# Kernel optimization log

Measured on AMD Instinct MI355X. Metric: run time of the kernel, lower is better.

## Reference

```python
import jax, jax.numpy as jnp
import numpy as np

B, S = 128, 1024
IN_NUM, IN_STATE = 64, 16
FEAT = 256
HID = 512
NUM_CLS = 32
EMB_WORD, EMB_DIM = 32, 4
LN_EPS = 1e-5


def _layer_norm(x):
    mu = jnp.mean(x, axis=-1, keepdims=True)
    var = jnp.var(x, axis=-1, keepdims=True)
    return (x - mu) * jax.lax.rsqrt(var + LN_EPS)


def setup_inputs() -> dict:
    key = jax.random.key(0)
    ks = jax.random.split(key, 20)
    w = lambda k, shape: jax.random.normal(k, shape, dtype=jnp.float32) * 0.05
    inp = {
        'x_num': jax.random.normal(ks[0], (B, S, IN_NUM), dtype=jnp.float32),
        'x_state': jax.random.randint(ks[1], (B, S, IN_STATE), 0, EMB_WORD),
        # numeric-branch MLP (2 layers)
        'num_w0': w(ks[2], (FEAT, IN_NUM)), 'num_b0': jnp.zeros((FEAT,), jnp.float32),
        'num_w1': w(ks[3], (FEAT, FEAT)),   'num_b1': jnp.zeros((FEAT,), jnp.float32),
        # state-branch embedding + MLP
        'emb': w(ks[4], (EMB_WORD, EMB_DIM)),
        'st_w0': w(ks[5], (FEAT, IN_STATE * EMB_DIM)), 'st_b0': jnp.zeros((FEAT,), jnp.float32),
        'st_w1': w(ks[6], (FEAT, FEAT)),               'st_b1': jnp.zeros((FEAT,), jnp.float32),
        # LSTM gate weights: input dim = 2*FEAT
        'Wii': w(ks[7], (HID, 2 * FEAT)),  'Whi': w(ks[8], (HID, HID)),
        'Wif': w(ks[9], (HID, 2 * FEAT)),  'Whf': w(ks[10], (HID, HID)),
        'Wig': w(ks[11], (HID, 2 * FEAT)), 'Whg': w(ks[12], (HID, HID)),
        'Wio': w(ks[13], (HID, 2 * FEAT)), 'Who': w(ks[14], (HID, HID)),
        'Bii': jnp.zeros((HID,), jnp.float32), 'Bhi': jnp.zeros((HID,), jnp.float32),
        'Bif': jnp.zeros((HID,), jnp.float32), 'Bhf': jnp.zeros((HID,), jnp.float32),
        'Big': jnp.zeros((HID,), jnp.float32), 'Bhg': jnp.zeros((HID,), jnp.float32),
        'Bio': jnp.zeros((HID,), jnp.float32), 'Bho': jnp.zeros((HID,), jnp.float32),
        'out_w': w(ks[15], (NUM_CLS, HID)), 'out_b': jnp.zeros((NUM_CLS,), jnp.float32),
    }
    return inp


def _forward(x_num, x_state, num_w0, num_b0, num_w1, num_b1, emb,
             st_w0, st_b0, st_w1, st_b1,
             Wii, Whi, Wif, Whf, Wig, Whg, Wio, Who,
             Bii, Bhi, Bif, Bhf, Big, Bhg, Bio, Bho,
             out_w, out_b):
    b, s = x_num.shape[0], x_num.shape[1]
    # numeric branch: Linear -> relu -> LayerNorm (dropout is identity in eval)
    h = _layer_norm(jax.nn.relu(x_num @ num_w0.T + num_b0))
    h = _layer_norm(jax.nn.relu(h @ num_w1.T + num_b1))
    # state branch: embedding lookup, flatten per step, then MLP
    e = emb[x_state].reshape(b, s, -1)                      # [B,S,IN_STATE*EMB_DIM]
    g = _layer_norm(jax.nn.relu(e @ st_w0.T + st_b0))
    g = _layer_norm(jax.nn.relu(g @ st_w1.T + st_b1))
    x = jnp.concatenate([h, g], axis=2)                     # [B,S,2*FEAT]

    hid = Whi.shape[0]
    h0 = jnp.zeros((b, hid), x.dtype)
    c0 = jnp.zeros((b, hid), x.dtype)

    def step(carry, x_t):
        h_t, c_t = carry
        i_t = jax.nn.sigmoid(x_t @ Wii.T + h_t @ Whi.T + Bii + Bhi)
        f_t = jax.nn.sigmoid(x_t @ Wif.T + h_t @ Whf.T + Bif + Bhf)
        g_t = jnp.tanh(x_t @ Wig.T + h_t @ Whg.T + Big + Bhg)
        o_t = jax.nn.sigmoid(x_t @ Wio.T + h_t @ Who.T + Bio + Bho)
        c_new = f_t * c_t + i_t * g_t
        h_new = o_t * jnp.tanh(c_new)
        return (h_new, c_new), None

    (h_last, _), _ = jax.lax.scan(step, (h0, c0), jnp.swapaxes(x, 0, 1))
    return h_last @ out_w.T + out_b                          # [B, num_cls]


def reference(x_num, x_state, num_w0, num_b0, num_w1, num_b1, emb,
              st_w0, st_b0, st_w1, st_b1,
              Wii, Whi, Wif, Whf, Wig, Whg, Wio, Who,
              Bii, Bhi, Bif, Bhf, Big, Bhg, Bio, Bho,
              out_w, out_b):
    return _forward(x_num, x_state, num_w0, num_b0, num_w1, num_b1, emb,
                    st_w0, st_b0, st_w1, st_b1,
                    Wii, Whi, Wif, Whf, Wig, Whg, Wio, Who,
                    Bii, Bhi, Bif, Bhf, Big, Bhg, Bio, Bho,
                    out_w, out_b)
```

## Files before the change

kernel.cpp:

```cpp
#include <hip/hip_runtime.h>
#include <hip/hip_bf16.h>

typedef __attribute__((ext_vector_type(4))) float f4;
typedef __attribute__((ext_vector_type(4))) float f32x4;
typedef __attribute__((ext_vector_type(8))) short bf16x8;
typedef unsigned long long ull;

#define OFF_XCAT   0ull
#define OFF_WCAT   134217728ull
#define OFF_BIAS   138412032ull
#define OFF_HBUF   138420224ull
#define OFF_FLAG   138682368ull
#define OFF_CTR    138686464ull
#define WS_NEED    138691584ull

__device__ inline unsigned short f2bf(float x){
  unsigned u = __float_as_uint(x);
  unsigned r = (u + 0x7FFFu + ((u >> 16) & 1u)) >> 16;
  return (unsigned short)r;
}
__device__ inline float bf2f(unsigned short s){ return __uint_as_float(((unsigned)s) << 16); }

__global__ void __launch_bounds__(256) diag_write(float* out, float val){
  out[blockIdx.x * 256 + threadIdx.x] = val;
}

__global__ void __launch_bounds__(256) prep_w(
    const float* Wii, const float* Wif, const float* Wig, const float* Wio,
    const float* Whi, const float* Whf, const float* Whg, const float* Who,
    const float* Bii, const float* Bif, const float* Big, const float* Bio,
    const float* Bhi, const float* Bhf, const float* Bhg, const float* Bho,
    unsigned short* Wcat, float* bias_cat){
  int e = blockIdx.x * 256 + threadIdx.x;
  int col = e >> 10, k = e & 1023;
  int u = col >> 2, g = col & 3;
  float v;
  if (k < 512){
    const float* p = (g==0)?Wii:((g==1)?Wif:((g==2)?Wig:Wio));
    v = p[u*512 + k];
  } else {
    const float* p = (g==0)?Whi:((g==1)?Whf:((g==2)?Whg:Who));
    v = p[u*512 + (k-512)];
  }
  Wcat[e] = f2bf(v);
  if (e < 2048){
    int u2 = e >> 2, g2 = e & 3;
    const float* bx = (g2==0)?Bii:((g2==1)?Bif:((g2==2)?Big:Bio));
    const float* bh = (g2==0)?Bhi:((g2==1)?Bhf:((g2==2)?Bhg:Bho));
    bias_cat[e] = bx[u2] + bh[u2];
  }
}

__global__ void __launch_bounds__(256) stageA_fused(
    const float* __restrict__ xnum, const int* __restrict__ xstate,
    const float* __restrict__ emb,
    const float* __restrict__ num_w0, const float* __restrict__ num_b0,
    const float* __restrict__ num_w1, const float* __restrict__ num_b1,
    const float* __restrict__ st_w0,  const float* __restrict__ st_b0,
    const float* __restrict__ st_w1,  const float* __restrict__ st_b1,
    unsigned short* __restrict__ Xcat){
  __shared__ float Wt[32*256];
  __shared__ float xb[16*68];
  __shared__ float h1[16*260];
  int tid = threadIdx.x;
  long tok0 = (long)blockIdx.x * 16;
  int tg = tid >> 6, c4 = tid & 63;

  #pragma unroll 1
  for (int br = 0; br < 2; ++br){
    const float* W0 = br ? st_w0 : num_w0;
    const float* b0 = br ? st_b0 : num_b0;
    const float* W1 = br ? st_w1 : num_w1;
    const float* b1 = br ? st_b1 : num_b1;

    __syncthreads();
    if (br == 0){
      int tk = tid >> 4, q = tid & 15;
      f4 v = *(const f4*)(xnum + (tok0+tk)*64 + q*4);
      float* d = xb + tk*68 + q*4;
      d[0]=v.x; d[1]=v.y; d[2]=v.z; d[3]=v.w;
    } else {
      int tk = tid >> 4, j = tid & 15;
      int idx = xstate[(tok0+tk)*16 + j];
      f4 v = *(const f4*)(emb + idx*4);
      float* d = xb + tk*68 + j*4;
      d[0]=v.x; d[1]=v.y; d[2]=v.z; d[3]=v.w;
    }

    float acc[4][4];
    { f4 bv = *(const f4*)(b0 + c4*4);
      #pragma unroll
      for (int j=0;j<4;j++){ acc[j][0]=bv.x; acc[j][1]=bv.y; acc[j][2]=bv.z; acc[j][3]=bv.w; } }
    for (int kh=0; kh<2; ++kh){
      __syncthreads();
      { int c = tid;
        const f4* src = (const f4*)(W0 + c*64 + kh*32);
        #pragma unroll
        for (int q=0;q<8;q++){
          f4 v = src[q];
          Wt[(q*4+0)*256 + c] = v.x; Wt[(q*4+1)*256 + c] = v.y;
          Wt[(q*4+2)*256 + c] = v.z; Wt[(q*4+3)*256 + c] = v.w;
        }
      }
      __syncthreads();
      for (int kq=0; kq<8; kq++){
        int k0 = kh*32 + kq*4;
        f4 a0 = *(const f4*)(xb + (tg*4+0)*68 + k0);
        f4 a1 = *(const f4*)(xb + (tg*4+1)*68 + k0);
        f4 a2 = *(const f4*)(xb + (tg*4+2)*68 + k0);
        f4 a3 = *(const f4*)(xb + (tg*4+3)*68 + k0);
        f4 w0 = *(const f4*)(Wt + (kq*4+0)*256 + c4*4);
        f4 w1 = *(const f4*)(Wt + (kq*4+1)*256 + c4*4);
        f4 w2 = *(const f4*)(Wt + (kq*4+2)*256 + c4*4);
        f4 w3 = *(const f4*)(Wt + (kq*4+3)*256 + c4*4);
        #pragma unroll
        for (int j=0;j<4;j++){
          f4 a = (j==0)?a0:((j==1)?a1:((j==2)?a2:a3));
          #pragma unroll
          for (int d=0; d<4; d++)
            acc[j][d] += a.x*w0[d] + a.y*w1[d] + a.z*w2[d] + a.w*w3[d];
        }
      }
    }
    #pragma unroll
    for (int j=0;j<4;j++){
      float v0=fmaxf(acc[j][0],0.f), v1=fmaxf(acc[j][1],0.f);
      float v2=fmaxf(acc[j][2],0.f), v3=fmaxf(acc[j][3],0.f);
      float s1 = v0+v1+v2+v3, s2 = v0*v0+v1*v1+v2*v2+v3*v3;
      for (int off=1; off<64; off<<=1){ s1 += __shfl_xor(s1, off); s2 += __shfl_xor(s2, off); }
      float mu = s1 * (1.f/256.f);
      float rs = rsqrtf(s2*(1.f/256.f) - mu*mu + 1e-5f);
      f4 o; o.x=(v0-mu)*rs; o.y=(v1-mu)*rs; o.z=(v2-mu)*rs; o.w=(v3-mu)*rs;
      *(f4*)(h1 + (tg*4+j)*260 + c4*4) = o;
    }

    float ac2[4][4];
    { f4 bv = *(const f4*)(b1 + c4*4);
      #pragma unroll
      for (int j=0;j<4;j++){ ac2[j][0]=bv.x; ac2[j][1]=bv.y; ac2[j][2]=bv.z; ac2[j][3]=bv.w; } }
    for (int kh=0; kh<8; ++kh){
      __syncthreads();
      { int c = tid;
        const f4* src = (const f4*)(W1 + c*256 + kh*32);
        #pragma unroll
        for (int q=0;q<8;q++){
          f4 v = src[q];
          Wt[(q*4+0)*256 + c] = v.x; Wt[(q*4+1)*256 + c] = v.y;
          Wt[(q*4+2)*256 + c] = v.z; Wt[(q*4+3)*256 + c] = v.w;
        }
      }
      __syncthreads();
      for (int kq=0; kq<8; kq++){
        int k0 = kh*32 + kq*4;
        f4 a0 = *(const f4*)(h1 + (tg*4+0)*260 + k0);
        f4 a1 = *(const f4*)(h1 + (tg*4+1)*260 + k0);
        f4 a2 = *(const f4*)(h1 + (tg*4+2)*260 + k0);
        f4 a3 = *(const f4*)(h1 + (tg*4+3)*260 + k0);
        f4 w0 = *(const f4*)(Wt + (kq*4+0)*256 + c4*4);
        f4 w1 = *(const f4*)(Wt + (kq*4+1)*256 + c4*4);
        f4 w2 = *(const f4*)(Wt + (kq*4+2)*256 + c4*4);
        f4 w3 = *(const f4*)(Wt + (kq*4+3)*256 + c4*4);
        #pragma unroll
        for (int j=0;j<4;j++){
          f4 a = (j==0)?a0:((j==1)?a1:((j==2)?a2:a3));
          #pragma unroll
          for (int d=0; d<4; d++)
            ac2[j][d] += a.x*w0[d] + a.y*w1[d] + a.z*w2[d] + a.w*w3[d];
        }
      }
    }
    #pragma unroll
    for (int j=0;j<4;j++){
      float v0=fmaxf(ac2[j][0],0.f), v1=fmaxf(ac2[j][1],0.f);
      float v2=fmaxf(ac2[j][2],0.f), v3=fmaxf(ac2[j][3],0.f);
      float s1 = v0+v1+v2+v3, s2 = v0*v0+v1*v1+v2*v2+v3*v3;
      for (int off=1; off<64; off<<=1){ s1 += __shfl_xor(s1, off); s2 += __shfl_xor(s2, off); }
      float mu = s1 * (1.f/256.f);
      float rs = rsqrtf(s2*(1.f/256.f) - mu*mu + 1e-5f);
      long tok = tok0 + tg*4 + j;
      long bb = tok >> 10, ss = tok & 1023;
      unsigned short* o = Xcat + (ss*128 + bb)*512 + br*256 + c4*4;
      unsigned lo = (unsigned)f2bf((v0-mu)*rs) | ((unsigned)f2bf((v1-mu)*rs) << 16);
      unsigned hi = (unsigned)f2bf((v2-mu)*rs) | ((unsigned)f2bf((v3-mu)*rs) << 16);
      ((unsigned*)o)[0] = lo; ((unsigned*)o)[1] = hi;
    }
  }
}

__global__ void __launch_bounds__(256, 1) lstm_pk(
    const unsigned short* __restrict__ Xcat,
    const unsigned short* __restrict__ Wcat,
    const float* __restrict__ bias_cat,
    unsigned int* __restrict__ hbuf32,
    unsigned int* __restrict__ flags,
    unsigned int* __restrict__ ctr){
  __shared__ __align__(16) char actb[32768];
  __shared__ int okf, sdead;
  int tid = threadIdx.x;
  int lane = tid & 63, w = tid >> 6;
  int g = blockIdx.x & 7, m = blockIdx.x >> 3;

  int colg = 64*m + 16*w + (lane & 15);
  bf16x8 wf[32];
  {
    const bf16x8* wsrc = (const bf16x8*)(Wcat + colg*1024 + (lane>>4)*8);
    #pragma unroll
    for (int s=0;s<32;s++) wf[s] = wsrc[s*4];
  }
  int cb = 64*m + 16*w + 4*(lane>>4);
  f32x4 bias4;
  bias4.x = bias_cat[cb+0]; bias4.y = bias_cat[cb+1];
  bias4.z = bias_cat[cb+2]; bias4.w = bias_cat[cb+3];

  if (tid == 0){
    __hip_atomic_fetch_add(&ctr[255], 1u, __ATOMIC_RELAXED, __HIP_MEMORY_SCOPE_AGENT);
    unsigned v = 0; int it = 0;
    do {
      v = __hip_atomic_load(&ctr[255], __ATOMIC_RELAXED, __HIP_MEMORY_SCOPE_AGENT);
      if (v >= 256u) break;
      __builtin_amdgcn_s_sleep(8);
    } while (++it < 2000000);
    okf = (v >= 256u) ? 1 : 0;
    sdead = 0;
  }
  __syncthreads();
  if (!okf) return;

  float cst = 0.f;
  int r16 = tid >> 4, q16 = tid & 15;
  const unsigned int* fl = flags + g*32;
  unsigned int* myflag = flags + g*32 + m;

  for (int t=0; t<1024; ++t){
    bf16x8 xf[16];
    {
      const bf16x8* xsrc = (const bf16x8*)(Xcat + ((long)t*128 + g*16 + (lane&15))*512 + (lane>>4)*8);
      #pragma unroll
      for (int s=0;s<16;s++) xf[s] = xsrc[s*4];
    }
    f32x4 acc0 = bias4;
    f32x4 acc1; acc1.x=0.f; acc1.y=0.f; acc1.z=0.f; acc1.w=0.f;
    #pragma unroll
    for (int s=0;s<16;s+=2){
      acc0 = __builtin_amdgcn_mfma_f32_16x16x32_bf16(wf[s],   xf[s],   acc0, 0, 0, 0);
      acc1 = __builtin_amdgcn_mfma_f32_16x16x32_bf16(wf[s+1], xf[s+1], acc1, 0, 0, 0);
    }
    if (t > 0 && w == 0){
      unsigned tt = (unsigned)t; int itc = 0;
      for (;;){
        unsigned a = __hip_atomic_load(&fl[lane & 31], __ATOMIC_RELAXED, __HIP_MEMORY_SCOPE_AGENT);
        if (__all((int)(a >= tt))) break;
        if (++itc > 400000){
          if (lane == 0){
            sdead = 1;
            __hip_atomic_store(&ctr[252], tt, __ATOMIC_RELAXED, __HIP_MEMORY_SCOPE_AGENT);
          }
          break;
        }
      }
      asm volatile("" ::: "memory");
    }
    __syncthreads();
    if (*(volatile int*)&sdead) break;
    {
      const ull* hb = (const ull*)hbuf32 + ((long)(t&1)*8 + g)*(16*128) + r16*128 + q16;
      char* hl = actb + (t&1)*16384;
      ull hv[8];
      #pragma unroll
      for (int i=0;i<8;i++)
        hv[i] = __hip_atomic_load(&hb[i*16], __ATOMIC_RELAXED, __HIP_MEMORY_SCOPE_AGENT);
      #pragma unroll
      for (int i=0;i<8;i++){
        int byt = (r16*1024 + q16*8 + i*128) ^ ((r16 & 7) << 4);
        *(ull*)(hl + byt) = hv[i];
      }
    }
    __syncthreads();
    {
      const char* hl = actb + (t&1)*16384;
      #pragma unroll
      for (int s=0;s<16;s+=2){
        int by0 = ((lane&15)*1024 + s*64     + (lane>>4)*16) ^ (((lane&15)&7) << 4);
        int by1 = ((lane&15)*1024 + (s+1)*64 + (lane>>4)*16) ^ (((lane&15)&7) << 4);
        bf16x8 b0 = *(const bf16x8*)(hl + by0);
        bf16x8 b1 = *(const bf16x8*)(hl + by1);
        acc0 = __builtin_amdgcn_mfma_f32_16x16x32_bf16(wf[16+s], b0, acc0, 0, 0, 0);
        acc1 = __builtin_amdgcn_mfma_f32_16x16x32_bf16(wf[17+s], b1, acc1, 0, 0, 0);
      }
    }
    float gi = acc0.x + acc1.x, gf = acc0.y + acc1.y;
    float gg = acc0.z + acc1.z, go = acc0.w + acc1.w;
    float iv = 1.f / (1.f + __expf(-gi));
    float fv = 1.f / (1.f + __expf(-gf));
    float e2 = __expf(-2.f * gg);
    float gv = (1.f - e2) / (1.f + e2);
    float ov = 1.f / (1.f + __expf(-go));
    cst = fv * cst + iv * gv;
    float e2c = __expf(-2.f * cst);
    float hout = ov * (1.f - e2c) / (1.f + e2c);
    {
      unsigned short hb16 = f2bf(hout);
      int partner = __shfl_xor((int)hb16, 16);
      int hi = lane >> 4;
      if ((hi & 1) == 0){
        int ug = 16*m + 4*w + hi;
        int r = lane & 15;
        unsigned pack = (unsigned)hb16 | (((unsigned)partner & 0xFFFFu) << 16);
        unsigned int* dst = hbuf32 + ((long)((t+1)&1)*8 + g)*(16*256) + r*256 + (ug >> 1);
        __hip_atomic_store(dst, pack, __ATOMIC_RELAXED, __HIP_MEMORY_SCOPE_AGENT);
      }
    }
    asm volatile("s_waitcnt vmcnt(0)" ::: "memory");
    __syncthreads();
    if (tid == 0)
      __hip_atomic_store(myflag, (unsigned)(t+1), __ATOMIC_RELAXED, __HIP_MEMORY_SCOPE_AGENT);
  }

  __syncthreads();
  if (tid == 0 && !sdead)
    __hip_atomic_fetch_add(&ctr[251], 1u, __ATOMIC_RELAXED, __HIP_MEMORY_SCOPE_AGENT);
}

__global__ void __launch_bounds__(256) out_gemm(
    const unsigned short* __restrict__ hbuf, const unsigned int* __restrict__ ctr,
    const float* __restrict__ out_w, const float* __restrict__ out_b,
    float* __restrict__ out){
  unsigned done = ctr[251], arriv = ctr[255], dead = ctr[252];
  if (dead != 0u || done != 256u){
    float v = dead ? (20000.f + (float)dead) : (10000.f + (float)arriv);
    if (threadIdx.x < 32) out[blockIdx.x*32 + threadIdx.x] = v;
    return;
  }
  __shared__ float part[8][32];
  int b = blockIdx.x;
  int g = b >> 4, r = b & 15;
  const unsigned short* hrow = hbuf + ((long)g*16 + r)*512;
  int col = threadIdx.x & 31, p = threadIdx.x >> 5;
  float s = 0.f;
  for (int u = p*64; u < p*64 + 64; ++u)
    s += bf2f(hrow[u]) * out_w[col*512 + u];
  part[p][col] = s;
  __syncthreads();
  if (p == 0){
    float t = out_b[col];
    #pragma unroll
    for (int i=0;i<8;i++) t += part[i][col];
    out[b*32 + col] = t;
  }
}

extern "C" void kernel_launch(void* const* d_in, const int* in_sizes, int n_in,
                              void* d_out, int out_size, void* d_ws, size_t ws_size,
                              hipStream_t stream){
  const float* x_num   = (const float*)d_in[0];
  const int*   x_state = (const int*)d_in[1];
  const float* num_w0  = (const float*)d_in[2];
  const float* num_b0  = (const float*)d_in[3];
  const float* num_w1  = (const float*)d_in[4];
  const float* num_b1  = (const float*)d_in[5];
  const float* emb     = (const float*)d_in[6];
  const float* st_w0   = (const float*)d_in[7];
  const float* st_b0   = (const float*)d_in[8];
  const float* st_w1   = (const float*)d_in[9];
  const float* st_b1   = (const float*)d_in[10];
  const float* Wii = (const float*)d_in[11];
  const float* Whi = (const float*)d_in[12];
  const float* Wif = (const float*)d_in[13];
  const float* Whf = (const float*)d_in[14];
  const float* Wig = (const float*)d_in[15];
  const float* Whg = (const float*)d_in[16];
  const float* Wio = (const float*)d_in[17];
  const float* Who = (const float*)d_in[18];
  const float* Bii = (const float*)d_in[19];
  const float* Bhi = (const float*)d_in[20];
  const float* Bif = (const float*)d_in[21];
  const float* Bhf = (const float*)d_in[22];
  const float* Big = (const float*)d_in[23];
  const float* Bhg = (const float*)d_in[24];
  const float* Bio = (const float*)d_in[25];
  const float* Bho = (const float*)d_in[26];
  const float* out_w = (const float*)d_in[27];
  const float* out_b = (const float*)d_in[28];

  float* out = (float*)d_out;

  diag_write<<<16, 256, 0, stream>>>(out, 50000.f);

  if (ws_size < WS_NEED){
    diag_write<<<16, 256, 0, stream>>>(out, 100000.f + (float)(ws_size >> 20));
    return;
  }

  char* ws = (char*)d_ws;
  unsigned short* Xcat = (unsigned short*)(ws + OFF_XCAT);
  unsigned short* Wcat = (unsigned short*)(ws + OFF_WCAT);
  float* bias_cat      = (float*)(ws + OFF_BIAS);
  unsigned int* hbuf32 = (unsigned int*)(ws + OFF_HBUF);
  unsigned int* flags  = (unsigned int*)(ws + OFF_FLAG);
  unsigned int* ctr    = (unsigned int*)(ws + OFF_CTR);

  hipMemsetAsync(ws + OFF_HBUF, 0, 262144 + 4096 + 1024, stream);

  prep_w<<<8192, 256, 0, stream>>>(Wii, Wif, Wig, Wio, Whi, Whf, Whg, Who,
                                   Bii, Bif, Big, Bio, Bhi, Bhf, Bhg, Bho,
                                   Wcat, bias_cat);

  stageA_fused<<<8192, 256, 0, stream>>>(x_num, x_state, emb,
                                         num_w0, num_b0, num_w1, num_b1,
                                         st_w0, st_b0, st_w1, st_b1, Xcat);

  lstm_pk<<<256, 256, 0, stream>>>(Xcat, Wcat, bias_cat, hbuf32, flags, ctr);

  out_gemm<<<128, 256, 0, stream>>>((const unsigned short*)hbuf32, ctr, out_w, out_b, out);
}
```

Before: 5.789 ms.

## Use per-wave flags and prefetch next step's input GEMM off the critical path

```diff
diff --git a/kernel.cpp b/kernel.cpp
--- a/kernel.cpp
+++ b/kernel.cpp
@@ -11,7 +11,7 @@
 #define OFF_BIAS   138412032ull
 #define OFF_HBUF   138420224ull
 #define OFF_FLAG   138682368ull
-#define OFF_CTR    138686464ull
+#define OFF_CTR    138690560ull
 #define WS_NEED    138691584ull
 
 __device__ inline unsigned short f2bf(float x){
@@ -192,7 +192,7 @@
     const unsigned short* __restrict__ Wcat,
     const float* __restrict__ bias_cat,
     unsigned int* __restrict__ hbuf32,
-    unsigned int* __restrict__ flags,
+    ull* __restrict__ flg,
     unsigned int* __restrict__ ctr){
   __shared__ __align__(16) char actb[32768];
   __shared__ int okf, sdead;
@@ -206,6 +206,8 @@
     const bf16x8* wsrc = (const bf16x8*)(Wcat + colg*1024 + (lane>>4)*8);
     #pragma unroll
     for (int s=0;s<32;s++) wf[s] = wsrc[s*4];
+    #pragma unroll
+    for (int s=0;s<32;s++) asm volatile("" : "+v"(wf[s]));
   }
   int cb = 64*m + 16*w + 4*(lane>>4);
   f32x4 bias4;
@@ -228,47 +230,48 @@
 
   float cst = 0.f;
   int r16 = tid >> 4, q16 = tid & 15;
-  const unsigned int* fl = flags + g*32;
-  unsigned int* myflag = flags + g*32 + m;
-
-  for (int t=0; t<1024; ++t){
+  ull* f8 = flg + g*128;
+  unsigned int* myflag = (unsigned int*)(f8 + (m*4 + w));
+
+  f32x4 acc0, acc1;
+  {
     bf16x8 xf[16];
-    {
-      const bf16x8* xsrc = (const bf16x8*)(Xcat + ((long)t*128 + g*16 + (lane&15))*512 + (lane>>4)*8);
-      #pragma unroll
-      for (int s=0;s<16;s++) xf[s] = xsrc[s*4];
-    }
-    f32x4 acc0 = bias4;
-    f32x4 acc1; acc1.x=0.f; acc1.y=0.f; acc1.z=0.f; acc1.w=0.f;
+    const bf16x8* xsrc = (const bf16x8*)(Xcat + ((long)0*128 + g*16 + (lane&15))*512 + (lane>>4)*8);
+    #pragma unroll
+    for (int s=0;s<16;s++) xf[s] = xsrc[s*4];
+    acc0 = bias4;
+    acc1.x=0.f; acc1.y=0.f; acc1.z=0.f; acc1.w=0.f;
     #pragma unroll
     for (int s=0;s<16;s+=2){
       acc0 = __builtin_amdgcn_mfma_f32_16x16x32_bf16(wf[s],   xf[s],   acc0, 0, 0, 0);
       acc1 = __builtin_amdgcn_mfma_f32_16x16x32_bf16(wf[s+1], xf[s+1], acc1, 0, 0, 0);
     }
-    if (t > 0 && w == 0){
+  }
+
+  #pragma unroll 1
+  for (int t=0; t<1024; ++t){
+    if (t > 0){
       unsigned tt = (unsigned)t; int itc = 0;
       for (;;){
-        unsigned a = __hip_atomic_load(&fl[lane & 31], __ATOMIC_RELAXED, __HIP_MEMORY_SCOPE_AGENT);
-        if (__all((int)(a >= tt))) break;
+        unsigned a = __hip_atomic_load((const unsigned int*)(f8 + lane),      __ATOMIC_RELAXED, __HIP_MEMORY_SCOPE_AGENT);
+        unsigned b = __hip_atomic_load((const unsigned int*)(f8 + 64 + lane), __ATOMIC_RELAXED, __HIP_MEMORY_SCOPE_AGENT);
+        if (__all((int)(a >= tt)) && __all((int)(b >= tt))) break;
+        if ((itc & 127) == 127 && *(volatile int*)&sdead) break;
         if (++itc > 400000){
-          if (lane == 0){
-            sdead = 1;
-            __hip_atomic_store(&ctr[252], tt, __ATOMIC_RELAXED, __HIP_MEMORY_SCOPE_AGENT);
-          }
+          *(volatile int*)&sdead = 1;
+          __hip_atomic_store(&ctr[252], tt, __ATOMIC_RELAXED, __HIP_MEMORY_SCOPE_AGENT);
           break;
         }
       }
       asm volatile("" ::: "memory");
     }
-    __syncthreads();
-    if (*(volatile int*)&sdead) break;
     {
       const ull* hb = (const ull*)hbuf32 + ((long)(t&1)*8 + g)*(16*128) + r16*128 + q16;
-      char* hl = actb + (t&1)*16384;
       ull hv[8];
       #pragma unroll
       for (int i=0;i<8;i++)
         hv[i] = __hip_atomic_load(&hb[i*16], __ATOMIC_RELAXED, __HIP_MEMORY_SCOPE_AGENT);
+      char* hl = actb + (t&1)*16384;
       #pragma unroll
       for (int i=0;i<8;i++){
         int byt = (r16*1024 + q16*8 + i*128) ^ ((r16 & 7) << 4);
@@ -276,6 +279,7 @@
       }
     }
     __syncthreads();
+    if (*(volatile int*)&sdead) break;
     {
       const char* hl = actb + (t&1)*16384;
       #pragma unroll
@@ -311,9 +315,22 @@
       }
     }
     asm volatile("s_waitcnt vmcnt(0)" ::: "memory");
-    __syncthreads();
-    if (tid == 0)
+    if (lane == 0)
       __hip_atomic_store(myflag, (unsigned)(t+1), __ATOMIC_RELAXED, __HIP_MEMORY_SCOPE_AGENT);
+    {
+      int tn = (t < 1023) ? (t+1) : 1023;
+      bf16x8 xf[16];
+      const bf16x8* xsrc = (const bf16x8*)(Xcat + ((long)tn*128 + g*16 + (lane&15))*512 + (lane>>4)*8);
+      #pragma unroll
+      for (int s=0;s<16;s++) xf[s] = xsrc[s*4];
+      acc0 = bias4;
+      acc1.x=0.f; acc1.y=0.f; acc1.z=0.f; acc1.w=0.f;
+      #pragma unroll
+      for (int s=0;s<16;s+=2){
+        acc0 = __builtin_amdgcn_mfma_f32_16x16x32_bf16(wf[s],   xf[s],   acc0, 0, 0, 0);
+        acc1 = __builtin_amdgcn_mfma_f32_16x16x32_bf16(wf[s+1], xf[s+1], acc1, 0, 0, 0);
+      }
+    }
   }
 
   __syncthreads();
@@ -396,10 +413,10 @@
   unsigned short* Wcat = (unsigned short*)(ws + OFF_WCAT);
   float* bias_cat      = (float*)(ws + OFF_BIAS);
   unsigned int* hbuf32 = (unsigned int*)(ws + OFF_HBUF);
-  unsigned int* flags  = (unsigned int*)(ws + OFF_FLAG);
+  ull* flg             = (ull*)(ws + OFF_FLAG);
   unsigned int* ctr    = (unsigned int*)(ws + OFF_CTR);
 
-  hipMemsetAsync(ws + OFF_HBUF, 0, 262144 + 4096 + 1024, stream);
+  hipMemsetAsync(ws + OFF_HBUF, 0, 262144 + 8192 + 1024, stream);
 
   prep_w<<<8192, 256, 0, stream>>>(Wii, Wif, Wig, Wio, Whi, Whf, Whg, Who,
                                    Bii, Bif, Big, Bio, Bhi, Bhf, Bhg, Bho,
@@ -409,7 +426,7 @@
                                          num_w0, num_b0, num_w1, num_b1,
                                          st_w0, st_b0, st_w1, st_b1, Xcat);
 
-  lstm_pk<<<256, 256, 0, stream>>>(Xcat, Wcat, bias_cat, hbuf32, flags, ctr);
+  lstm_pk<<<256, 256, 0, stream>>>(Xcat, Wcat, bias_cat, hbuf32, flg, ctr);
 
   out_gemm<<<128, 256, 0, stream>>>((const unsigned short*)hbuf32, ctr, out_w, out_b, out);
 }
```

Result: faster. 5.467 ms (-5.6%).
